# Kernel optimization log

Measured on AMD Instinct MI355X. Metric: run time of the kernel, lower is better.

## Reference

```python
import jax, jax.numpy as jnp
import numpy as np

NEG = -1e30  # stand-in for -inf that keeps logaddexp grad-safe


def _ctc_neg_log_likelihood(predictions, labels):
    # predictions: [B, T, C] logits; labels: [B, L] int, -1 = padding.
    # tf.nn.ctc_loss(blank_index=-1) => blank class is C-1.
    B, T, C = predictions.shape
    L = labels.shape[1]
    S = 2 * L + 1
    blank = C - 1

    label_len = jnp.sum((labels != -1).astype(jnp.int32), axis=-1)  # [B]
    labels_c = jnp.where(labels < 0, 0, labels).astype(jnp.int32)

    # Extended label sequence: blank, l1, blank, l2, ..., blank  -> [B, S]
    ext = jnp.full((B, S), blank, dtype=jnp.int32)
    ext = ext.at[:, 1::2].set(labels_c)

    # s-2 transition allowed only at label positions (odd s) with ext[s] != ext[s-2]
    same = jnp.concatenate([jnp.zeros((B, 2), bool), ext[:, 2:] == ext[:, :-2]], axis=1)
    is_label_pos = (jnp.arange(S) % 2 == 1)[None, :]
    allow2 = is_label_pos & ~same  # [B, S]

    # valid extended positions per example: s < 2*label_len + 1
    valid = jnp.arange(S)[None, :] < (2 * label_len + 1)[:, None]  # [B, S]

    log_probs = jax.nn.log_softmax(predictions, axis=-1)  # [B, T, C]
    # emission log-prob for each extended-label slot: [B, T, S]
    lp_ext = jnp.take_along_axis(log_probs, jnp.broadcast_to(ext[:, None, :], (B, T, S)), axis=2)

    has_lab = label_len > 0
    alpha0 = jnp.full((B, S), NEG, dtype=log_probs.dtype)
    alpha0 = alpha0.at[:, 0].set(lp_ext[:, 0, 0])
    alpha0 = alpha0.at[:, 1].set(jnp.where(has_lab, lp_ext[:, 0, 1], NEG))
    alpha0 = jnp.where(valid, alpha0, NEG)

    def step(alpha, lp_t):
        a1 = alpha
        a2 = jnp.pad(alpha, ((0, 0), (1, 0)), constant_values=NEG)[:, :S]
        a3 = jnp.pad(alpha, ((0, 0), (2, 0)), constant_values=NEG)[:, :S]
        a3 = jnp.where(allow2, a3, NEG)
        new = jnp.logaddexp(jnp.logaddexp(a1, a2), a3) + lp_t
        new = jnp.where(valid, new, NEG)
        return new, None

    lp_rest = jnp.moveaxis(lp_ext[:, 1:], 1, 0)  # [T-1, B, S]
    alphaT, _ = jax.lax.scan(step, alpha0, lp_rest)

    idx1 = (2 * label_len)[:, None]              # final blank
    idx2 = jnp.maximum(idx1 - 1, 0)              # final label
    a_end1 = jnp.take_along_axis(alphaT, idx1, axis=1)[:, 0]
    a_end2 = jnp.take_along_axis(alphaT, idx2, axis=1)[:, 0]
    a_end2 = jnp.where(has_lab, a_end2, NEG)
    log_lik = jnp.logaddexp(a_end1, a_end2)
    return -log_lik  # [B]


def setup_inputs() -> dict:
    key = jax.random.key(0)
    k1, k2 = jax.random.split(key)
    B, T, C, L = 1024, 384, 96, 48
    labels = jax.random.randint(k1, (B, L), 0, C - 1).astype(jnp.int64)
    predictions = jax.random.normal(k2, (B, T, C), dtype=jnp.float32)
    return {"labels": labels, "predictions": predictions}


def reference(labels, predictions):
    per_example = _ctc_neg_log_likelihood(predictions, labels)
    return jnp.mean(per_example)
```

## Files before the change

kernel.cpp:

```cpp
#include <hip/hip_runtime.h>

constexpr int Tt = 384;
constexpr int Cc = 96;
constexpr int Ll = 48;
constexpr int Gg = 8;
constexpr int NG = 24;
constexpr int RS = 128;

#define L2E 1.4426950408889634f
#define LN2 0.6931471805599453f
#define LNEG (-3.0e38f)

template <int CTRL, int RM = 0xF>
__device__ __forceinline__ float dppf(float x) {
    return __int_as_float(
        __builtin_amdgcn_update_dpp(0, __float_as_int(x), CTRL, RM, 0xF, true));
}
template <int CTRL>
__device__ __forceinline__ int dppi(int x) {
    return __builtin_amdgcn_update_dpp(0, x, CTRL, 0xF, 0xF, true);
}
__device__ __forceinline__ float bcast63(float x) {
    return __int_as_float(__builtin_amdgcn_readlane(__float_as_int(x), 63));
}
__device__ __forceinline__ float wsum(float x) {
    x += dppf<0x111>(x);
    x += dppf<0x112>(x);
    x += dppf<0x114>(x);
    x += dppf<0x118>(x);
    x += dppf<0x142, 0xA>(x);
    x += dppf<0x143, 0xC>(x);
    return bcast63(x);
}
__device__ __forceinline__ float shup1(float x) { return dppf<0x138>(x); }
__device__ __forceinline__ float shdn1(float x) { return dppf<0x130>(x); }
__device__ __forceinline__ float exp2i(int d) {
    d = d < -126 ? -126 : (d > 126 ? 126 : d);
    return __int_as_float((d + 127) << 23);
}

template <bool FWD>
__device__ __forceinline__ void prod_load(const float2* __restrict__ rp2, float2* q,
                                          int g, int lane) {
#pragma unroll
    for (int j = 0; j < Gg; ++j) {
        int k = g * Gg + j;
        int t = FWD ? k : (Tt - 1 - k);
        q[j] = (lane < 48) ? rp2[(size_t)t * 48 + lane] : make_float2(-1e4f, -1e4f);
    }
}
__device__ __forceinline__ void prod_group(const float2* q, float* dst, int lane) {
#pragma unroll
    for (int j = 0; j < Gg; ++j) {
        float ex = __builtin_amdgcn_exp2f(q[j].x * L2E);
        float ey = __builtin_amdgcn_exp2f(q[j].y * L2E);
        float s  = wsum(ex + ey);
        float rZ = __builtin_amdgcn_rcpf(s);
        ((float2*)(dst + j * RS))[lane] = make_float2(ex * rZ, ey * rZ);
    }
}

template <bool FWD>
__device__ __forceinline__ void dp_group(const float* __restrict__ pr, int labv,
                                         float allow2f, float& st_e, float& st_o,
                                         int& ls, float& f, float& a2f) {
    float plC[Gg], pbC[Gg];
#pragma unroll
    for (int j = 0; j < Gg; ++j) {
        plC[j] = pr[j * RS + labv];
        pbC[j] = pr[j * RS + 95];
    }
#pragma unroll
    for (int j = 0; j < Gg; ++j) {
        if (FWD) {
            float sh = shup1(st_o);
            float t0 = st_e + st_o;
            float ne = fmaf(f, sh, st_e) * pbC[j];
            float no = fmaf(a2f, sh, t0) * plC[j];
            st_e = ne; st_o = no;
        } else {
            float en = shdn1(st_e);
            float on = shdn1(st_o);
            float ne = (st_e + st_o) * pbC[j];
            float no = fmaf(a2f, on, fmaf(f, en, st_o)) * plC[j];
            st_e = ne; st_o = no;
        }
    }
    float m = fmaxf(st_e, st_o);
    bool z  = (m == 0.0f);
    int eb  = (__float_as_int(m) >> 23) & 0xFF;
    eb = eb > 253 ? 253 : eb;
    float r = z ? 1.0f : __int_as_float((254 - eb) << 23);
    st_e *= r; st_o *= r;
    ls += z ? 0 : (eb - 127);
#pragma unroll
    for (int it = 0; it < 8; ++it) {
        int lsn = FWD ? dppi<0x138>(ls) : dppi<0x130>(ls);
        ls = z ? lsn : ls;
    }
    int lsn2 = FWD ? dppi<0x138>(ls) : dppi<0x130>(ls);
    f   = exp2i(lsn2 - ls);
    a2f = allow2f * f;
}

__global__ __launch_bounds__(64) void zero_kernel(float* o) { *o = 0.0f; }

__global__ __launch_bounds__(256) void ctc_fb(const int* __restrict__ labels,
                                              const float* __restrict__ pred,
                                              float* __restrict__ out,
                                              float invB) {
    const int b    = blockIdx.x;
    const int lane = threadIdx.x & 63;
    const int wv   = threadIdx.x >> 6;
    const float2* rp2 = (const float2*)(pred + (size_t)b * Tt * Cc);

    __shared__ float plb[2][2][Gg][RS];
    __shared__ float sbe[64], sbo[64];
    __shared__ int   slsb[64];

    int v = (lane < Ll) ? labels[(size_t)b * Ll + lane] : -1;
    int present = (lane < Ll) && (v != -1);
    int labv = (v < 0) ? 0 : v;
    unsigned long long pm = __ballot(present);
    int len = __popcll(pm);
    int lab_p = __shfl(labv, (lane - 1) & 63, 64);
    int lab_n = __shfl(labv, (lane + 1) & 63, 64);

    float st_e = 0.0f, st_o = 0.0f, f = 1.0f, a2f = 0.0f, allow2f = 0.0f;
    int   ls = 0;
    float2 qA[Gg], qB[Gg];

    if (wv == 0) {
        allow2f = (lane >= 1 && labv != lab_p) ? 1.0f : 0.0f;
        st_e = (lane == 0) ? 1.0f : 0.0f;
        a2f = allow2f;
    } else if (wv == 1) {
        allow2f = (labv != lab_n) ? 1.0f : 0.0f;
        st_e = (lane == len) ? 1.0f : 0.0f;
        a2f = allow2f;
    } else if (wv == 2) {
        prod_load<true>(rp2, qA, 0, lane);
        prod_load<true>(rp2, qB, 1, lane);
    } else {
        prod_load<false>(rp2, qA, 0, lane);
        prod_load<false>(rp2, qB, 1, lane);
    }

    for (int i = 0; i <= NG; ++i) {
        if (wv == 2 && i < NG) {
            if ((i & 1) == 0) {
                prod_group(qA, &plb[0][0][0][0], lane);
                if (i + 2 < NG) prod_load<true>(rp2, qA, i + 2, lane);
            } else {
                prod_group(qB, &plb[0][1][0][0], lane);
                if (i + 2 < NG) prod_load<true>(rp2, qB, i + 2, lane);
            }
        } else if (wv == 3 && i < NG) {
            if ((i & 1) == 0) {
                prod_group(qA, &plb[1][0][0][0], lane);
                if (i + 2 < NG) prod_load<false>(rp2, qA, i + 2, lane);
            } else {
                prod_group(qB, &plb[1][1][0][0], lane);
                if (i + 2 < NG) prod_load<false>(rp2, qB, i + 2, lane);
            }
        } else if (wv == 0 && i >= 1) {
            dp_group<true>(&plb[0][(i - 1) & 1][0][0], labv, allow2f, st_e, st_o, ls, f, a2f);
        } else if (wv == 1 && i >= 1) {
            dp_group<false>(&plb[1][(i - 1) & 1][0][0], labv, allow2f, st_e, st_o, ls, f, a2f);
        }
        __syncthreads();
    }

    if (wv == 1) {
        sbe[lane]  = st_e;
        sbo[lane]  = st_o;
        slsb[lane] = ls;
    }
    __syncthreads();

    if (wv == 0) {
        float sh  = shup1(st_o);
        int   lsu = dppi<0x138>(ls);
        float fup = exp2i(lsu - ls);
        float Ae = fmaf(fup, sh, st_e);
        float Ao = fmaf(allow2f * fup, sh, st_e + st_o);
        float be = sbe[lane], bo = sbo[lane];
        float base = (float)(ls + slsb[lane]);
        float l1 = (Ae > 0.0f && be > 0.0f) ? __log2f(Ae) + __log2f(be) + base : LNEG;
        float l2 = (Ao > 0.0f && bo > 0.0f) ? __log2f(Ao) + __log2f(bo) + base : LNEG;
        float mm = fmaxf(l1, l2);
#pragma unroll
        for (int off = 32; off >= 1; off >>= 1) mm = fmaxf(mm, __shfl_xor(mm, off, 64));
        float ss = exp2f(l1 - mm) + exp2f(l2 - mm);
#pragma unroll
        for (int off = 32; off >= 1; off >>= 1) ss += __shfl_xor(ss, off, 64);
        if (lane == 0) {
            float ll = (mm + __log2f(ss)) * LN2;
            atomicAdd(out, -ll * invB);
        }
    }
}

extern "C" void kernel_launch(void* const* d_in, const int* in_sizes, int n_in,
                              void* d_out, int out_size, void* d_ws, size_t ws_size,
                              hipStream_t stream) {
    const int*   labels = (const int*)d_in[0];
    const float* pred   = (const float*)d_in[1];
    float*       out    = (float*)d_out;

    const int B = in_sizes[0] / Ll;

    hipLaunchKernelGGL(zero_kernel, dim3(1), dim3(64), 0, stream, out);
    hipLaunchKernelGGL(ctc_fb, dim3(B), dim3(256), 0, stream,
                       labels, pred, out, 1.0f / (float)B);
}
```

Measured before the change: 223.9 us.

## Fuse softmax producer into DP waves, dropping shared-memory handoff and barriers

Removes the separate producer waves and the LDS double buffer. Each DP wave (forward and backward) now loads its own logits, computes the softmax normalizer, and gathers the label and blank probabilities through cross-lane shuffles into registers. It then software-pipelines the load and softmax of the next group against the DP of the current group. This eliminates the per-group __syncthreads and LDS traffic and halves the block size to 128 threads. In exchange, each DP wave does more serial work on its critical path and uses more registers.

```diff
diff --git a/kernel.cpp b/kernel.cpp
--- a/kernel.cpp
+++ b/kernel.cpp
@@ -5,7 +5,6 @@
 constexpr int Ll = 48;
 constexpr int Gg = 8;
 constexpr int NG = 24;
-constexpr int RS = 128;
 
 #define L2E 1.4426950408889634f
 #define LN2 0.6931471805599453f
@@ -49,40 +48,40 @@
         q[j] = (lane < 48) ? rp2[(size_t)t * 48 + lane] : make_float2(-1e4f, -1e4f);
     }
 }
-__device__ __forceinline__ void prod_group(const float2* q, float* dst, int lane) {
+
+__device__ __forceinline__ void softmax_group(const float2* q, float* pl, float* pb,
+                                              int idx_h, int bitsel) {
 #pragma unroll
     for (int j = 0; j < Gg; ++j) {
         float ex = __builtin_amdgcn_exp2f(q[j].x * L2E);
         float ey = __builtin_amdgcn_exp2f(q[j].y * L2E);
+        float gb = __shfl(ey, 47, 64);
+        float g0 = __shfl(ex, idx_h, 64);
+        float g1 = __shfl(ey, idx_h, 64);
         float s  = wsum(ex + ey);
         float rZ = __builtin_amdgcn_rcpf(s);
-        ((float2*)(dst + j * RS))[lane] = make_float2(ex * rZ, ey * rZ);
+        pl[j] = (bitsel ? g1 : g0) * rZ;
+        pb[j] = gb * rZ;
     }
 }
 
 template <bool FWD>
-__device__ __forceinline__ void dp_group(const float* __restrict__ pr, int labv,
+__device__ __forceinline__ void dp_group(const float* pl, const float* pb,
                                          float allow2f, float& st_e, float& st_o,
                                          int& ls, float& f, float& a2f) {
-    float plC[Gg], pbC[Gg];
-#pragma unroll
-    for (int j = 0; j < Gg; ++j) {
-        plC[j] = pr[j * RS + labv];
-        pbC[j] = pr[j * RS + 95];
-    }
 #pragma unroll
     for (int j = 0; j < Gg; ++j) {
         if (FWD) {
             float sh = shup1(st_o);
             float t0 = st_e + st_o;
-            float ne = fmaf(f, sh, st_e) * pbC[j];
-            float no = fmaf(a2f, sh, t0) * plC[j];
+            float ne = fmaf(f, sh, st_e) * pb[j];
+            float no = fmaf(a2f, sh, t0) * pl[j];
             st_e = ne; st_o = no;
         } else {
             float en = shdn1(st_e);
             float on = shdn1(st_o);
-            float ne = (st_e + st_o) * pbC[j];
-            float no = fmaf(a2f, on, fmaf(f, en, st_o)) * plC[j];
+            float ne = (st_e + st_o) * pb[j];
+            float no = fmaf(a2f, on, fmaf(f, en, st_o)) * pl[j];
             st_e = ne; st_o = no;
         }
     }
@@ -103,9 +102,30 @@
     a2f = allow2f * f;
 }
 
+template <bool FWD>
+__device__ __forceinline__ void run_half(const float2* __restrict__ rp2, int lane,
+                                         int idx_h, int bitsel, float allow2f,
+                                         float& st_e, float& st_o, int& ls,
+                                         float& f, float& a2f) {
+    float2 q0[Gg], q1[Gg];
+    float plA[Gg], pbA[Gg], plB[Gg], pbB[Gg];
+    prod_load<FWD>(rp2, q0, 0, lane);
+    prod_load<FWD>(rp2, q1, 1, lane);
+    softmax_group(q0, plA, pbA, idx_h, bitsel);
+    for (int g2 = 0; g2 < NG / 2; ++g2) {
+        bool more = (g2 < NG / 2 - 1);
+        if (more) prod_load<FWD>(rp2, q0, 2 * g2 + 2, lane);
+        softmax_group(q1, plB, pbB, idx_h, bitsel);
+        dp_group<FWD>(plA, pbA, allow2f, st_e, st_o, ls, f, a2f);
+        if (more) prod_load<FWD>(rp2, q1, 2 * g2 + 3, lane);
+        if (more) softmax_group(q0, plA, pbA, idx_h, bitsel);
+        dp_group<FWD>(plB, pbB, allow2f, st_e, st_o, ls, f, a2f);
+    }
+}
+
 __global__ __launch_bounds__(64) void zero_kernel(float* o) { *o = 0.0f; }
 
-__global__ __launch_bounds__(256) void ctc_fb(const int* __restrict__ labels,
+__global__ __launch_bounds__(128) void ctc_fb(const int* __restrict__ labels,
                                               const float* __restrict__ pred,
                                               float* __restrict__ out,
                                               float invB) {
@@ -114,7 +134,6 @@
     const int wv   = threadIdx.x >> 6;
     const float2* rp2 = (const float2*)(pred + (size_t)b * Tt * Cc);
 
-    __shared__ float plb[2][2][Gg][RS];
     __shared__ float sbe[64], sbo[64];
     __shared__ int   slsb[64];
 
@@ -123,55 +142,24 @@
     int labv = (v < 0) ? 0 : v;
     unsigned long long pm = __ballot(present);
     int len = __popcll(pm);
+    int idx_h  = labv >> 1;
+    int bitsel = labv & 1;
     int lab_p = __shfl(labv, (lane - 1) & 63, 64);
     int lab_n = __shfl(labv, (lane + 1) & 63, 64);
 
-    float st_e = 0.0f, st_o = 0.0f, f = 1.0f, a2f = 0.0f, allow2f = 0.0f;
+    float st_e, st_o = 0.0f, f = 1.0f, a2f, allow2f;
     int   ls = 0;
-    float2 qA[Gg], qB[Gg];
 
     if (wv == 0) {
         allow2f = (lane >= 1 && labv != lab_p) ? 1.0f : 0.0f;
         st_e = (lane == 0) ? 1.0f : 0.0f;
         a2f = allow2f;
-    } else if (wv == 1) {
+        run_half<true>(rp2, lane, idx_h, bitsel, allow2f, st_e, st_o, ls, f, a2f);
+    } else {
         allow2f = (labv != lab_n) ? 1.0f : 0.0f;
         st_e = (lane == len) ? 1.0f : 0.0f;
         a2f = allow2f;
-    } else if (wv == 2) {
-        prod_load<true>(rp2, qA, 0, lane);
-        prod_load<true>(rp2, qB, 1, lane);
-    } else {
-        prod_load<false>(rp2, qA, 0, lane);
-        prod_load<false>(rp2, qB, 1, lane);
-    }
-
-    for (int i = 0; i <= NG; ++i) {
-        if (wv == 2 && i < NG) {
-            if ((i & 1) == 0) {
-                prod_group(qA, &plb[0][0][0][0], lane);
-                if (i + 2 < NG) prod_load<true>(rp2, qA, i + 2, lane);
-            } else {
-                prod_group(qB, &plb[0][1][0][0], lane);
-                if (i + 2 < NG) prod_load<true>(rp2, qB, i + 2, lane);
-            }
-        } else if (wv == 3 && i < NG) {
-            if ((i & 1) == 0) {
-                prod_group(qA, &plb[1][0][0][0], lane);
-                if (i + 2 < NG) prod_load<false>(rp2, qA, i + 2, lane);
-            } else {
-                prod_group(qB, &plb[1][1][0][0], lane);
-                if (i + 2 < NG) prod_load<false>(rp2, qB, i + 2, lane);
-            }
-        } else if (wv == 0 && i >= 1) {
-            dp_group<true>(&plb[0][(i - 1) & 1][0][0], labv, allow2f, st_e, st_o, ls, f, a2f);
-        } else if (wv == 1 && i >= 1) {
-            dp_group<false>(&plb[1][(i - 1) & 1][0][0], labv, allow2f, st_e, st_o, ls, f, a2f);
-        }
-        __syncthreads();
-    }
-
-    if (wv == 1) {
+        run_half<false>(rp2, lane, idx_h, bitsel, allow2f, st_e, st_o, ls, f, a2f);
         sbe[lane]  = st_e;
         sbo[lane]  = st_o;
         slsb[lane] = ls;
@@ -211,6 +199,6 @@
     const int B = in_sizes[0] / Ll;
 
     hipLaunchKernelGGL(zero_kernel, dim3(1), dim3(64), 0, stream, out);
-    hipLaunchKernelGGL(ctc_fb, dim3(B), dim3(256), 0, stream,
+    hipLaunchKernelGGL(ctc_fb, dim3(B), dim3(128), 0, stream,
                        labels, pred, out, 1.0f / (float)B);
 }
```

After: 223.3 us. Within noise of the previous version (-0.3%).
